# Kernel tuning notes

Measured on AMD Instinct MI355X. Metric: run time of the kernel, lower is better.

The kernel has to match this reference:

```python
import jax, jax.numpy as jnp
import numpy as np

N_NODES = 100000
N_EDGES = 1600000
IN_DIM, HID_DIM, OUT_DIM = 128, 64, 1


def gcn_conv(x, W, b, src, dst, num_nodes):
    """PyG-style GCNConv: h = x @ W, symmetric deg^-1/2 normalization,
    scatter-add aggregation at dst, plus bias. src/dst already include self-loops."""
    h = x @ W  # [N, out]
    ones = jnp.ones(src.shape[0], dtype=h.dtype)
    deg = jax.ops.segment_sum(ones, dst, num_segments=num_nodes)  # in-degree incl. self-loop
    dinv = jnp.where(deg > 0, jax.lax.rsqrt(deg), 0.0)
    norm = dinv[src] * dinv[dst]  # [E+N]
    msg = h[src] * norm[:, None]  # gather + scale  [E+N, out]
    out = jax.ops.segment_sum(msg, dst, num_segments=num_nodes)  # scatter-add
    return out + b


def setup_inputs() -> dict:
    key = jax.random.key(0)
    k_x, k_e, k_w1, k_w2 = jax.random.split(key, 4)
    x = jax.random.normal(k_x, (N_NODES, IN_DIM), dtype=jnp.float32)
    edge_index = jax.random.randint(k_e, (2, N_EDGES), 0, N_NODES, dtype=jnp.int64)
    # Glorot-ish init for linear weights
    W1 = jax.random.normal(k_w1, (IN_DIM, HID_DIM), dtype=jnp.float32) / np.sqrt(IN_DIM)
    b1 = jnp.zeros((HID_DIM,), dtype=jnp.float32)
    W2 = jax.random.normal(k_w2, (HID_DIM, OUT_DIM), dtype=jnp.float32) / np.sqrt(HID_DIM)
    b2 = jnp.zeros((OUT_DIM,), dtype=jnp.float32)
    return {"x": x, "edge_index": edge_index, "W1": W1, "b1": b1, "W2": W2, "b2": b2}


def reference(x, edge_index, W1, b1, W2, b2):
    N = x.shape[0]
    loop = jnp.arange(N, dtype=edge_index.dtype)  # self-loops (GCNConv default)
    src = jnp.concatenate([edge_index[0], loop])
    dst = jnp.concatenate([edge_index[1], loop])
    h = jax.nn.relu(gcn_conv(x, W1, b1, src, dst, N))
    out = gcn_conv(h, W2, b2, src, dst, N)
    return jax.nn.sigmoid(out)
```

## Files before the change

### kernel.cpp

```cpp
#include <hip/hip_runtime.h>
#include <math.h>

#define NBINS 512
#define CAPB  4800

typedef __attribute__((ext_vector_type(8))) short bf16x8;
typedef __attribute__((ext_vector_type(4))) float f32x4;

union Fu { float f; unsigned u; };
__device__ inline unsigned short bhi(float f) { Fu v; v.f = f; return (unsigned short)(v.u >> 16); }
__device__ inline float bup(unsigned short h) { Fu v; v.u = ((unsigned)h) << 16; return v.f; }
__device__ inline float flo(unsigned d) { Fu v; v.u = d << 16; return v.f; }
__device__ inline float fhi(unsigned d) { Fu v; v.u = d & 0xffff0000u; return v.f; }

__global__ __launch_bounds__(256) void k_prep(const float* __restrict__ W1,
                                              unsigned short* __restrict__ w1h,
                                              unsigned short* __restrict__ w1l,
                                              int* __restrict__ bcursor) {
    int t = threadIdx.x;
    if (blockIdx.x == 34) {
        bcursor[t] = t * CAPB;
        bcursor[t + 256] = (t + 256) * CAPB;
        return;
    }
    int i = blockIdx.x * 256 + t;
    int n = i / 136, c = i - n * 136;
    unsigned short hh = 0, ll = 0;
    if (c < 128) {
        float f = W1[c * 64 + n];
        hh = bhi(f);
        ll = bhi(f - bup(hh));
    }
    w1h[i] = hh;
    w1l[i] = ll;
}

__global__ __launch_bounds__(256) void k_bscatter(const int* __restrict__ src,
                                                  const int* __restrict__ dst,
                                                  int* __restrict__ bcursor,
                                                  unsigned int* __restrict__ ebuf,
                                                  int E) {
    __shared__ int lh[NBINS];
    __shared__ int lbase[NBINS];
    for (int i = threadIdx.x; i < NBINS; i += 256) lh[i] = 0;
    __syncthreads();
    int base = blockIdx.x * 4096;
    int t = threadIdx.x;
    int s_[16], d_[16], r_[16];
#pragma unroll
    for (int k = 0; k < 16; ++k) {
        int e = base + k * 256 + t;
        if (e < E) {
            int dd = dst[e];
            d_[k] = dd;
            s_[k] = src[e];
            r_[k] = atomicAdd(&lh[dd >> 8], 1);
        }
    }
    __syncthreads();
    for (int i = threadIdx.x; i < NBINS; i += 256) {
        int c = lh[i];
        lbase[i] = c ? atomicAdd(&bcursor[i], c) : 0;
    }
    __syncthreads();
#pragma unroll
    for (int k = 0; k < 16; ++k) {
        int e = base + k * 256 + t;
        if (e < E) {
            int b = d_[k] >> 8;
            int p = lbase[b] + r_[k];
            if (p < (b + 1) * CAPB)
                ebuf[p] = ((unsigned int)(d_[k] & 255) << 24) | (unsigned int)s_[k];
        }
    }
}

__global__ __launch_bounds__(256) void k_bucket_csr(const unsigned int* __restrict__ ebuf,
                                                    const int* __restrict__ bcursor,
                                                    int* __restrict__ rowptr,
                                                    int* __restrict__ degs,
                                                    float* __restrict__ dinv,
                                                    int* __restrict__ col,
                                                    int N) {
    __shared__ unsigned int se[CAPB];
    __shared__ int lh[256];
    __shared__ int lex[256];
    __shared__ int lcur[256];
    int b = blockIdx.x;
    int t = threadIdx.x;
    int beg = b * CAPB;
    int end = bcursor[b];
    if (end > beg + CAPB) end = beg + CAPB;
    int cnt = end - beg;
    lh[t] = 0;
    __syncthreads();
    for (int i = t; i < cnt; i += 256) {
        unsigned int v = ebuf[beg + i];
        se[i] = v;
        atomicAdd(&lh[v >> 24], 1);
    }
    __syncthreads();
    lex[t] = lh[t];
    __syncthreads();
    for (int off = 1; off < 256; off <<= 1) {
        int x = lex[t];
        int y = (t >= off) ? lex[t - off] : 0;
        __syncthreads();
        lex[t] = x + y;
        __syncthreads();
    }
    int excl = lex[t] - lh[t];
    int node = (b << 8) + t;
    if (node < N) {
        rowptr[node] = beg + excl;
        degs[node] = lh[t];
        dinv[node] = rsqrtf((float)(lh[t] + 1));
    }
    lcur[t] = beg + excl;
    __syncthreads();
    for (int i = t; i < cnt; i += 256) {
        unsigned int v = se[i];
        int p = atomicAdd(&lcur[v >> 24], 1);
        col[p] = (int)(v & 0xFFFFFF);
    }
}

__global__ __launch_bounds__(256) void k_gemm1m(const float* __restrict__ x,
                                                const unsigned short* __restrict__ w1h,
                                                const unsigned short* __restrict__ w1l,
                                                const float* __restrict__ dinv,
                                                unsigned short* __restrict__ h1b, int N) {
    __shared__ __align__(16) unsigned short Wh[64 * 136];
    __shared__ __align__(16) unsigned short Wl[64 * 136];

    int tid = threadIdx.x;
    int base = blockIdx.x * 64;

    for (int i = tid; i < 1088; i += 256) {
        ((bf16x8*)Wh)[i] = ((const bf16x8*)w1h)[i];
        ((bf16x8*)Wl)[i] = ((const bf16x8*)w1l)[i];
    }
    __syncthreads();

    int l = tid & 63, wv = tid >> 6;
    int lr = l & 15, lg = l >> 4;

    int arow = base + 16 * wv + lr;
    if (arow >= N) arow = N - 1;
    const float* xr = x + (size_t)arow * 128 + lg * 8;

    f32x4 acc[4];
#pragma unroll
    for (int nt = 0; nt < 4; ++nt) acc[nt] = (f32x4){0.f, 0.f, 0.f, 0.f};

    int boff = lr * 136 + lg * 8;
#pragma unroll
    for (int s = 0; s < 4; ++s) {
        float4 va = *(const float4*)(xr + s * 32);
        float4 vb = *(const float4*)(xr + s * 32 + 4);
        float f[8] = {va.x, va.y, va.z, va.w, vb.x, vb.y, vb.z, vb.w};
        bf16x8 ah, al;
#pragma unroll
        for (int j = 0; j < 8; ++j) {
            unsigned short hh = bhi(f[j]);
            ah[j] = (short)hh;
            al[j] = (short)bhi(f[j] - bup(hh));
        }
#pragma unroll
        for (int nt = 0; nt < 4; ++nt) {
            bf16x8 bh = *(const bf16x8*)&Wh[boff + nt * 16 * 136 + s * 32];
            bf16x8 bl = *(const bf16x8*)&Wl[boff + nt * 16 * 136 + s * 32];
            acc[nt] = __builtin_amdgcn_mfma_f32_16x16x32_bf16(ah, bh, acc[nt], 0, 0, 0);
            acc[nt] = __builtin_amdgcn_mfma_f32_16x16x32_bf16(al, bh, acc[nt], 0, 0, 0);
            acc[nt] = __builtin_amdgcn_mfma_f32_16x16x32_bf16(ah, bl, acc[nt], 0, 0, 0);
        }
    }

    int m0 = base + 16 * wv + lg * 4;
#pragma unroll
    for (int reg = 0; reg < 4; ++reg) {
        int r = m0 + reg;
        if (r <= N) {
            float dv = (r < N) ? dinv[r] : 0.0f;
            unsigned short* op = h1b + (((size_t)r) << 6) + lr;
#pragma unroll
            for (int nt = 0; nt < 4; ++nt)
                op[nt * 16] = bhi(acc[nt][reg] * dv);
        }
    }
}

__global__ __launch_bounds__(256) void k_gather1(const unsigned short* __restrict__ h1b,
                                                 const int* __restrict__ rowptr,
                                                 const int* __restrict__ degs,
                                                 const int* __restrict__ col,
                                                 const float* __restrict__ dinv,
                                                 const float* __restrict__ b1,
                                                 const float* __restrict__ W2,
                                                 float* __restrict__ h2s, int N) {
    int lane = threadIdx.x & 63;
    int wv = threadIdx.x >> 6;
    int ns = lane >> 3, fg = lane & 7;
    int fgo = fg * 8;

    int d = (blockIdx.x * 4 + wv) * 8 + ns;
    bool dvalid = (d < N);
    int dd = dvalid ? d : N - 1;
    int beg = rowptr[dd];
    int deg = dvalid ? degs[dd] : 0;

    int maxd = deg;
#pragma unroll
    for (int off = 8; off < 64; off <<= 1)
        maxd = max(maxd, __shfl_xor(maxd, off));

    uint4 sv = *(const uint4*)&h1b[((size_t)dd << 6) + fgo];
    float acc[8];
    acc[0] = flo(sv.x); acc[1] = fhi(sv.x);
    acc[2] = flo(sv.y); acc[3] = fhi(sv.y);
    acc[4] = flo(sv.z); acc[5] = fhi(sv.z);
    acc[6] = flo(sv.w); acc[7] = fhi(sv.w);

    for (int it = 0; it < maxd; it += 16) {
        int s[16];
#pragma unroll
        for (int j = 0; j < 16; ++j) {
            int i = it + j;
            int c = col[beg + i];
            s[j] = (i < deg) ? c : N;
        }
        uint4 v[16];
#pragma unroll
        for (int j = 0; j < 16; ++j)
            v[j] = *(const uint4*)&h1b[((size_t)s[j] << 6) + fgo];
#pragma unroll
        for (int j = 0; j < 16; ++j) {
            acc[0] += flo(v[j].x); acc[1] += fhi(v[j].x);
            acc[2] += flo(v[j].y); acc[3] += fhi(v[j].y);
            acc[4] += flo(v[j].z); acc[5] += fhi(v[j].z);
            acc[6] += flo(v[j].w); acc[7] += fhi(v[j].w);
        }
    }

    const float4 b1a = *(const float4*)(b1 + fgo);
    const float4 b1b = *(const float4*)(b1 + fgo + 4);
    const float4 w2a = *(const float4*)(W2 + fgo);
    const float4 w2b = *(const float4*)(W2 + fgo + 4);
    float dv = dvalid ? dinv[d] : 0.0f;
    float p = 0.f;
    p += fmaxf(fmaf(acc[0], dv, b1a.x), 0.f) * w2a.x;
    p += fmaxf(fmaf(acc[1], dv, b1a.y), 0.f) * w2a.y;
    p += fmaxf(fmaf(acc[2], dv, b1a.z), 0.f) * w2a.z;
    p += fmaxf(fmaf(acc[3], dv, b1a.w), 0.f) * w2a.w;
    p += fmaxf(fmaf(acc[4], dv, b1b.x), 0.f) * w2b.x;
    p += fmaxf(fmaf(acc[5], dv, b1b.y), 0.f) * w2b.y;
    p += fmaxf(fmaf(acc[6], dv, b1b.z), 0.f) * w2b.z;
    p += fmaxf(fmaf(acc[7], dv, b1b.w), 0.f) * w2b.w;
    p += __shfl_xor(p, 1);
    p += __shfl_xor(p, 2);
    p += __shfl_xor(p, 4);
    if (fg == 0 && dvalid) h2s[d] = p * dv;
}

__global__ __launch_bounds__(256) void k_gather2(const float* __restrict__ h2s,
                                                 const int* __restrict__ rowptr,
                                                 const int* __restrict__ degs,
                                                 const int* __restrict__ col,
                                                 const float* __restrict__ dinv,
                                                 const float* __restrict__ b2,
                                                 float* __restrict__ out, int N) {
    int d = blockIdx.x * 256 + threadIdx.x;
    if (d >= N) return;
    float acc = h2s[d];
    int beg = rowptr[d];
    int deg = degs[d];
    for (int e = 0; e < deg; e += 8) {
        float s = 0.f;
#pragma unroll
        for (int j = 0; j < 8; ++j) {
            int i = e + j;
            float v = h2s[col[beg + min(i, deg - 1)]];
            s += (i < deg) ? v : 0.f;
        }
        acc += s;
    }
    float v = fmaf(acc, dinv[d], b2[0]);
    out[d] = 1.0f / (1.0f + expf(-v));
}

extern "C" void kernel_launch(void* const* d_in, const int* in_sizes, int n_in,
                              void* d_out, int out_size, void* d_ws, size_t ws_size,
                              hipStream_t stream) {
    const float* x  = (const float*)d_in[0];
    const int*   ei = (const int*)d_in[1];
    const float* W1 = (const float*)d_in[2];
    const float* b1 = (const float*)d_in[3];
    const float* W2 = (const float*)d_in[4];
    const float* b2 = (const float*)d_in[5];
    float* out = (float*)d_out;

    int N = in_sizes[0] / 128;
    int E = in_sizes[1] / 2;
    const int* src = ei;
    const int* dst = ei + E;

    char* w = (char*)d_ws;
    size_t region0 = (size_t)(N + 1) * 64 * 2;
    size_t ebytes  = (size_t)NBINS * CAPB * 4;
    if (ebytes > region0) region0 = ebytes;
    region0 = (region0 + 255) & ~(size_t)255;

    unsigned short* h1b = (unsigned short*)w;
    unsigned int* ebuf  = (unsigned int*)w;
    int* colv   = (int*)(w + region0);
    int* rowptr = colv + (size_t)NBINS * CAPB;
    size_t Npad = ((size_t)N + 511) & ~(size_t)511;
    int* degs   = rowptr + Npad;
    float* dinv = (float*)(degs + Npad);
    float* h2s  = dinv + Npad;
    int* bcursor = (int*)(h2s + Npad);
    unsigned short* w1h = (unsigned short*)(bcursor + NBINS + 8);
    unsigned short* w1l = w1h + 64 * 136;

    int nbuck = (N + 255) >> 8;

    k_prep      <<<35, 256, 0, stream>>>(W1, w1h, w1l, bcursor);
    k_bscatter  <<<(E + 4095) / 4096, 256, 0, stream>>>(src, dst, bcursor, ebuf, E);
    k_bucket_csr<<<nbuck, 256, 0, stream>>>(ebuf, bcursor, rowptr, degs, dinv, colv, N);
    k_gemm1m    <<<N / 64 + 1, 256, 0, stream>>>(x, w1h, w1l, dinv, h1b, N);
    k_gather1   <<<(N + 31) / 32, 256, 0, stream>>>(h1b, rowptr, degs, colv, dinv, b1, W2, h2s, N);
    k_gather2   <<<(N + 255) / 256, 256, 0, stream>>>(h2s, rowptr, degs, colv, dinv, b2, out, N);
}
```

Baseline: 101.6 us.

## Fuse edge bucket scatter with layer-1 GEMM and move source dinv scaling into gather

The edge bucket scatter and the x@W1 MFMA GEMM now run as two block ranges inside one launch, so the GEMM no longer waits on dinv from the CSR build and both overlap on the GPU. Because of that, h1 is stored unscaled and the gather applies dinv[src] per edge with an FMA, plus dinv[dst] for the self-loop term. The edge buffer gets its own workspace region instead of aliasing h1b. In exchange, the gather does an extra dependent dinv load per edge before the row fetch, and the combined kernel's shared-memory size is set by the GEMM path.

```diff
diff --git a/kernel.cpp b/kernel.cpp
--- a/kernel.cpp
+++ b/kernel.cpp
@@ -35,42 +35,110 @@
     w1l[i] = ll;
 }
 
-__global__ __launch_bounds__(256) void k_bscatter(const int* __restrict__ src,
-                                                  const int* __restrict__ dst,
-                                                  int* __restrict__ bcursor,
-                                                  unsigned int* __restrict__ ebuf,
-                                                  int E) {
-    __shared__ int lh[NBINS];
-    __shared__ int lbase[NBINS];
-    for (int i = threadIdx.x; i < NBINS; i += 256) lh[i] = 0;
-    __syncthreads();
-    int base = blockIdx.x * 4096;
+__global__ __launch_bounds__(256) void k_scat_gemm(const int* __restrict__ src,
+                                                   const int* __restrict__ dst,
+                                                   int* __restrict__ bcursor,
+                                                   unsigned int* __restrict__ ebuf,
+                                                   int E, int nsc,
+                                                   const float* __restrict__ x,
+                                                   const unsigned short* __restrict__ w1h,
+                                                   const unsigned short* __restrict__ w1l,
+                                                   unsigned short* __restrict__ h1b, int N) {
+    __shared__ __align__(16) char smem[34816];
     int t = threadIdx.x;
-    int s_[16], d_[16], r_[16];
-#pragma unroll
-    for (int k = 0; k < 16; ++k) {
-        int e = base + k * 256 + t;
-        if (e < E) {
-            int dd = dst[e];
-            d_[k] = dd;
-            s_[k] = src[e];
-            r_[k] = atomicAdd(&lh[dd >> 8], 1);
-        }
-    }
-    __syncthreads();
-    for (int i = threadIdx.x; i < NBINS; i += 256) {
-        int c = lh[i];
-        lbase[i] = c ? atomicAdd(&bcursor[i], c) : 0;
-    }
-    __syncthreads();
-#pragma unroll
-    for (int k = 0; k < 16; ++k) {
-        int e = base + k * 256 + t;
-        if (e < E) {
-            int b = d_[k] >> 8;
-            int p = lbase[b] + r_[k];
-            if (p < (b + 1) * CAPB)
-                ebuf[p] = ((unsigned int)(d_[k] & 255) << 24) | (unsigned int)s_[k];
+    if (blockIdx.x < nsc) {
+        int* lh = (int*)smem;
+        int* lbase = lh + NBINS;
+        for (int i = t; i < NBINS; i += 256) lh[i] = 0;
+        __syncthreads();
+        int base = blockIdx.x * 4096;
+        int s_[16], d_[16], r_[16];
+#pragma unroll
+        for (int k = 0; k < 16; ++k) {
+            int e = base + k * 256 + t;
+            if (e < E) {
+                int dd = dst[e];
+                d_[k] = dd;
+                s_[k] = src[e];
+                r_[k] = atomicAdd(&lh[dd >> 8], 1);
+            }
+        }
+        __syncthreads();
+        for (int i = t; i < NBINS; i += 256) {
+            int c = lh[i];
+            lbase[i] = c ? atomicAdd(&bcursor[i], c) : 0;
+        }
+        __syncthreads();
+#pragma unroll
+        for (int k = 0; k < 16; ++k) {
+            int e = base + k * 256 + t;
+            if (e < E) {
+                int b = d_[k] >> 8;
+                int p = lbase[b] + r_[k];
+                if (p < (b + 1) * CAPB)
+                    ebuf[p] = ((unsigned int)(d_[k] & 255) << 24) | (unsigned int)s_[k];
+            }
+        }
+    } else {
+        unsigned short* Wh = (unsigned short*)smem;
+        unsigned short* Wl = Wh + 64 * 136;
+        for (int i = t; i < 1088; i += 256) {
+            ((bf16x8*)Wh)[i] = ((const bf16x8*)w1h)[i];
+            ((bf16x8*)Wl)[i] = ((const bf16x8*)w1l)[i];
+        }
+        __syncthreads();
+
+        int base = (blockIdx.x - nsc) * 64;
+        int l = t & 63, wv = t >> 6;
+        int lr = l & 15, lg = l >> 4;
+
+        int arow = base + 16 * wv + lr;
+        if (arow >= N) arow = N - 1;
+        const float* xr = x + (size_t)arow * 128 + lg * 8;
+
+        f32x4 acc[4];
+#pragma unroll
+        for (int nt = 0; nt < 4; ++nt) acc[nt] = (f32x4){0.f, 0.f, 0.f, 0.f};
+
+        int boff = lr * 136 + lg * 8;
+#pragma unroll
+        for (int s = 0; s < 4; ++s) {
+            float4 va = *(const float4*)(xr + s * 32);
+            float4 vb = *(const float4*)(xr + s * 32 + 4);
+            float f[8] = {va.x, va.y, va.z, va.w, vb.x, vb.y, vb.z, vb.w};
+            bf16x8 ah, al;
+#pragma unroll
+            for (int j = 0; j < 8; ++j) {
+                unsigned short hh = bhi(f[j]);
+                ah[j] = (short)hh;
+                al[j] = (short)bhi(f[j] - bup(hh));
+            }
+#pragma unroll
+            for (int nt = 0; nt < 4; ++nt) {
+                bf16x8 bh = *(const bf16x8*)&Wh[boff + nt * 16 * 136 + s * 32];
+                bf16x8 bl = *(const bf16x8*)&Wl[boff + nt * 16 * 136 + s * 32];
+                acc[nt] = __builtin_amdgcn_mfma_f32_16x16x32_bf16(ah, bh, acc[nt], 0, 0, 0);
+                acc[nt] = __builtin_amdgcn_mfma_f32_16x16x32_bf16(al, bh, acc[nt], 0, 0, 0);
+                acc[nt] = __builtin_amdgcn_mfma_f32_16x16x32_bf16(ah, bl, acc[nt], 0, 0, 0);
+            }
+        }
+
+        int m0 = base + 16 * wv + lg * 4;
+#pragma unroll
+        for (int reg = 0; reg < 4; ++reg) {
+            int r = m0 + reg;
+            if (r <= N) {
+                unsigned short* op = h1b + (((size_t)r) << 6) + lr;
+                if (r < N) {
+#pragma unroll
+                    for (int nt = 0; nt < 4; ++nt)
+                        op[nt * 16] = bhi(acc[nt][reg]);
+                } else {
+#pragma unroll
+                    for (int nt = 0; nt < 4; ++nt)
+                        op[nt * 16] = 0;
+                }
+            }
         }
     }
 }
@@ -125,71 +193,6 @@
     }
 }
 
-__global__ __launch_bounds__(256) void k_gemm1m(const float* __restrict__ x,
-                                                const unsigned short* __restrict__ w1h,
-                                                const unsigned short* __restrict__ w1l,
-                                                const float* __restrict__ dinv,
-                                                unsigned short* __restrict__ h1b, int N) {
-    __shared__ __align__(16) unsigned short Wh[64 * 136];
-    __shared__ __align__(16) unsigned short Wl[64 * 136];
-
-    int tid = threadIdx.x;
-    int base = blockIdx.x * 64;
-
-    for (int i = tid; i < 1088; i += 256) {
-        ((bf16x8*)Wh)[i] = ((const bf16x8*)w1h)[i];
-        ((bf16x8*)Wl)[i] = ((const bf16x8*)w1l)[i];
-    }
-    __syncthreads();
-
-    int l = tid & 63, wv = tid >> 6;
-    int lr = l & 15, lg = l >> 4;
-
-    int arow = base + 16 * wv + lr;
-    if (arow >= N) arow = N - 1;
-    const float* xr = x + (size_t)arow * 128 + lg * 8;
-
-    f32x4 acc[4];
-#pragma unroll
-    for (int nt = 0; nt < 4; ++nt) acc[nt] = (f32x4){0.f, 0.f, 0.f, 0.f};
-
-    int boff = lr * 136 + lg * 8;
-#pragma unroll
-    for (int s = 0; s < 4; ++s) {
-        float4 va = *(const float4*)(xr + s * 32);
-        float4 vb = *(const float4*)(xr + s * 32 + 4);
-        float f[8] = {va.x, va.y, va.z, va.w, vb.x, vb.y, vb.z, vb.w};
-        bf16x8 ah, al;
-#pragma unroll
-        for (int j = 0; j < 8; ++j) {
-            unsigned short hh = bhi(f[j]);
-            ah[j] = (short)hh;
-            al[j] = (short)bhi(f[j] - bup(hh));
-        }
-#pragma unroll
-        for (int nt = 0; nt < 4; ++nt) {
-            bf16x8 bh = *(const bf16x8*)&Wh[boff + nt * 16 * 136 + s * 32];
-            bf16x8 bl = *(const bf16x8*)&Wl[boff + nt * 16 * 136 + s * 32];
-            acc[nt] = __builtin_amdgcn_mfma_f32_16x16x32_bf16(ah, bh, acc[nt], 0, 0, 0);
-            acc[nt] = __builtin_amdgcn_mfma_f32_16x16x32_bf16(al, bh, acc[nt], 0, 0, 0);
-            acc[nt] = __builtin_amdgcn_mfma_f32_16x16x32_bf16(ah, bl, acc[nt], 0, 0, 0);
-        }
-    }
-
-    int m0 = base + 16 * wv + lg * 4;
-#pragma unroll
-    for (int reg = 0; reg < 4; ++reg) {
-        int r = m0 + reg;
-        if (r <= N) {
-            float dv = (r < N) ? dinv[r] : 0.0f;
-            unsigned short* op = h1b + (((size_t)r) << 6) + lr;
-#pragma unroll
-            for (int nt = 0; nt < 4; ++nt)
-                op[nt * 16] = bhi(acc[nt][reg] * dv);
-        }
-    }
-}
-
 __global__ __launch_bounds__(256) void k_gather1(const unsigned short* __restrict__ h1b,
                                                  const int* __restrict__ rowptr,
                                                  const int* __restrict__ degs,
@@ -208,6 +211,7 @@
     int dd = dvalid ? d : N - 1;
     int beg = rowptr[dd];
     int deg = dvalid ? degs[dd] : 0;
+    float dvd = dvalid ? dinv[d] : 0.0f;
 
     int maxd = deg;
 #pragma unroll
@@ -216,18 +220,22 @@
 
     uint4 sv = *(const uint4*)&h1b[((size_t)dd << 6) + fgo];
     float acc[8];
-    acc[0] = flo(sv.x); acc[1] = fhi(sv.x);
-    acc[2] = flo(sv.y); acc[3] = fhi(sv.y);
-    acc[4] = flo(sv.z); acc[5] = fhi(sv.z);
-    acc[6] = flo(sv.w); acc[7] = fhi(sv.w);
+    acc[0] = flo(sv.x) * dvd; acc[1] = fhi(sv.x) * dvd;
+    acc[2] = flo(sv.y) * dvd; acc[3] = fhi(sv.y) * dvd;
+    acc[4] = flo(sv.z) * dvd; acc[5] = fhi(sv.z) * dvd;
+    acc[6] = flo(sv.w) * dvd; acc[7] = fhi(sv.w) * dvd;
 
     for (int it = 0; it < maxd; it += 16) {
         int s[16];
+        float w[16];
 #pragma unroll
         for (int j = 0; j < 16; ++j) {
             int i = it + j;
             int c = col[beg + i];
-            s[j] = (i < deg) ? c : N;
+            bool val = (i < deg);
+            int cc = val ? c : 0;
+            s[j] = val ? c : N;
+            w[j] = val ? dinv[cc] : 0.0f;
         }
         uint4 v[16];
 #pragma unroll
@@ -235,10 +243,10 @@
             v[j] = *(const uint4*)&h1b[((size_t)s[j] << 6) + fgo];
 #pragma unroll
         for (int j = 0; j < 16; ++j) {
-            acc[0] += flo(v[j].x); acc[1] += fhi(v[j].x);
-            acc[2] += flo(v[j].y); acc[3] += fhi(v[j].y);
-            acc[4] += flo(v[j].z); acc[5] += fhi(v[j].z);
-            acc[6] += flo(v[j].w); acc[7] += fhi(v[j].w);
+            acc[0] = fmaf(w[j], flo(v[j].x), acc[0]); acc[1] = fmaf(w[j], fhi(v[j].x), acc[1]);
+            acc[2] = fmaf(w[j], flo(v[j].y), acc[2]); acc[3] = fmaf(w[j], fhi(v[j].y), acc[3]);
+            acc[4] = fmaf(w[j], flo(v[j].z), acc[4]); acc[5] = fmaf(w[j], fhi(v[j].z), acc[5]);
+            acc[6] = fmaf(w[j], flo(v[j].w), acc[6]); acc[7] = fmaf(w[j], fhi(v[j].w), acc[7]);
         }
     }
 
@@ -246,20 +254,19 @@
     const float4 b1b = *(const float4*)(b1 + fgo + 4);
     const float4 w2a = *(const float4*)(W2 + fgo);
     const float4 w2b = *(const float4*)(W2 + fgo + 4);
-    float dv = dvalid ? dinv[d] : 0.0f;
     float p = 0.f;
-    p += fmaxf(fmaf(acc[0], dv, b1a.x), 0.f) * w2a.x;
-    p += fmaxf(fmaf(acc[1], dv, b1a.y), 0.f) * w2a.y;
-    p += fmaxf(fmaf(acc[2], dv, b1a.z), 0.f) * w2a.z;
-    p += fmaxf(fmaf(acc[3], dv, b1a.w), 0.f) * w2a.w;
-    p += fmaxf(fmaf(acc[4], dv, b1b.x), 0.f) * w2b.x;
-    p += fmaxf(fmaf(acc[5], dv, b1b.y), 0.f) * w2b.y;
-    p += fmaxf(fmaf(acc[6], dv, b1b.z), 0.f) * w2b.z;
-    p += fmaxf(fmaf(acc[7], dv, b1b.w), 0.f) * w2b.w;
+    p += fmaxf(fmaf(acc[0], dvd, b1a.x), 0.f) * w2a.x;
+    p += fmaxf(fmaf(acc[1], dvd, b1a.y), 0.f) * w2a.y;
+    p += fmaxf(fmaf(acc[2], dvd, b1a.z), 0.f) * w2a.z;
+    p += fmaxf(fmaf(acc[3], dvd, b1a.w), 0.f) * w2a.w;
+    p += fmaxf(fmaf(acc[4], dvd, b1b.x), 0.f) * w2b.x;
+    p += fmaxf(fmaf(acc[5], dvd, b1b.y), 0.f) * w2b.y;
+    p += fmaxf(fmaf(acc[6], dvd, b1b.z), 0.f) * w2b.z;
+    p += fmaxf(fmaf(acc[7], dvd, b1b.w), 0.f) * w2b.w;
     p += __shfl_xor(p, 1);
     p += __shfl_xor(p, 2);
     p += __shfl_xor(p, 4);
-    if (fg == 0 && dvalid) h2s[d] = p * dv;
+    if (fg == 0 && dvalid) h2s[d] = p * dvd;
 }
 
 __global__ __launch_bounds__(256) void k_gather2(const float* __restrict__ h2s,
@@ -305,14 +312,11 @@
     const int* dst = ei + E;
 
     char* w = (char*)d_ws;
-    size_t region0 = (size_t)(N + 1) * 64 * 2;
-    size_t ebytes  = (size_t)NBINS * CAPB * 4;
-    if (ebytes > region0) region0 = ebytes;
-    region0 = (region0 + 255) & ~(size_t)255;
+    size_t h1bytes = (((size_t)(N + 1) * 128) + 255) & ~(size_t)255;
 
     unsigned short* h1b = (unsigned short*)w;
-    unsigned int* ebuf  = (unsigned int*)w;
-    int* colv   = (int*)(w + region0);
+    unsigned int* ebuf  = (unsigned int*)(w + h1bytes);
+    int* colv   = (int*)((char*)ebuf + (size_t)NBINS * CAPB * 4);
     int* rowptr = colv + (size_t)NBINS * CAPB;
     size_t Npad = ((size_t)N + 511) & ~(size_t)511;
     int* degs   = rowptr + Npad;
@@ -323,11 +327,13 @@
     unsigned short* w1l = w1h + 64 * 136;
 
     int nbuck = (N + 255) >> 8;
+    int nsc   = (E + 4095) / 4096;
+    int ngemm = N / 64 + 1;
 
     k_prep      <<<35, 256, 0, stream>>>(W1, w1h, w1l, bcursor);
-    k_bscatter  <<<(E + 4095) / 4096, 256, 0, stream>>>(src, dst, bcursor, ebuf, E);
+    k_scat_gemm <<<nsc + ngemm, 256, 0, stream>>>(src, dst, bcursor, ebuf, E, nsc,
+                                                  x, w1h, w1l, h1b, N);
     k_bucket_csr<<<nbuck, 256, 0, stream>>>(ebuf, bcursor, rowptr, degs, dinv, colv, N);
-    k_gemm1m    <<<N / 64 + 1, 256, 0, stream>>>(x, w1h, w1l, dinv, h1b, N);
     k_gather1   <<<(N + 31) / 32, 256, 0, stream>>>(h1b, rowptr, degs, colv, dinv, b1, W2, h2s, N);
     k_gather2   <<<(N + 255) / 256, 256, 0, stream>>>(h2s, rowptr, degs, colv, dinv, b2, out, N);
 }
```

Result: slower. 108.7 us (+7.0%).
